# Kernel optimization log

Measured on AMD Instinct MI355X. Metric: run time of the kernel, lower is better.

The kernel has to match this reference:

```python
import jax, jax.numpy as jnp
import numpy as np

N = 100_000      # nodes
E = 1_600_000    # edges
F_IN = 128       # n_features == conv_dim1..3
F_OUT = 256      # concat_dim
G = 2000         # number of graphs in the batch
EPS = 1e-5       # BatchNorm eps


def _xavier(k, shape):
    fan_in, fan_out = shape[-2], shape[-1]
    lim = float(np.sqrt(6.0 / (fan_in + fan_out)))
    return jax.random.uniform(k, shape, jnp.float32, -lim, lim)


def setup_inputs() -> dict:
    key = jax.random.key(0)
    ks = jax.random.split(key, 8)
    x = jax.random.normal(ks[0], (N, F_IN), jnp.float32)
    edge_index = jax.random.randint(ks[1], (2, E), 0, N, dtype=jnp.int64)
    batch = jnp.sort(jax.random.randint(ks[2], (N,), 0, G, dtype=jnp.int64))
    # layers 1..5: F_IN -> F_IN (stacked), layer 6: F_IN -> F_OUT
    Wi = _xavier(ks[3], (5, F_IN, F_IN))   # ARMA init_weight per layer
    Wr = _xavier(ks[4], (5, F_IN, F_IN))   # ARMA root_weight per layer
    b = jnp.zeros((5, F_IN), jnp.float32)  # ARMA bias per layer
    g = jnp.ones((5, F_IN), jnp.float32)   # BN gamma
    be = jnp.zeros((5, F_IN), jnp.float32) # BN beta
    Wi6 = _xavier(ks[5], (F_IN, F_OUT))
    Wr6 = _xavier(ks[6], (F_IN, F_OUT))
    b6 = jnp.zeros((F_OUT,), jnp.float32)
    g6 = jnp.ones((F_OUT,), jnp.float32)
    be6 = jnp.zeros((F_OUT,), jnp.float32)
    return dict(x=x, edge_index=edge_index, batch=batch, Wi=Wi, Wr=Wr, b=b,
                g=g, be=be, Wi6=Wi6, Wr6=Wr6, b6=b6, g6=g6, be6=be6)


def _arma(x, norm, row, col, Wi_l, Wr_l, b_l):
    # ARMAConv (num_stacks=1, num_layers=1, act=ReLU):
    #   out = ReLU( A_norm @ (x W_init) + x W_root + b )
    h = x @ Wi_l                                           # [N, F_out]
    msg = h[row] * norm[:, None]                           # gather + scale, [E, F_out]
    agg = jax.ops.segment_sum(msg, col, num_segments=N)    # scatter-add
    return jax.nn.relu(agg + x @ Wr_l + b_l)


def _bn(x, gamma, beta):
    # BatchNorm1d, training mode (biased batch variance)
    mu = x.mean(axis=0)
    var = x.var(axis=0)
    return gamma * (x - mu) * jax.lax.rsqrt(var + EPS) + beta


def reference(x, edge_index, batch, Wi, Wr, b, g, be, Wi6, Wr6, b6, g6, be6):
    row, col = edge_index[0], edge_index[1]
    # gcn_norm without self loops: D^-1/2 A D^-1/2 edge weights
    deg = jax.ops.segment_sum(jnp.ones((E,), x.dtype), col, num_segments=N)
    dinv = jnp.where(deg > 0, jax.lax.rsqrt(deg), 0.0)
    norm = dinv[row] * dinv[col]                           # [E]

    h = x
    for l in range(5):  # fixed small layer count
        h = _arma(h, norm, row, col, Wi[l], Wr[l], b[l])   # outer F.relu is idempotent
        h = _bn(h, g[l], be[l])
    h = _arma(h, norm, row, col, Wi6, Wr6, b6)
    h = _bn(h, g6, be6)
    # global_add_pool over graph ids; dropout = identity (deterministic baseline)
    out = jax.ops.segment_sum(h, batch, num_segments=G)    # [G, F_OUT]
    return out
```

## Files before the change

### kernel.cpp

```cpp
#include <hip/hip_runtime.h>

#define Nn 100000
#define Ee 1600000
#define Gg 2000
#define EPSf 1e-5f

typedef unsigned short ushort_t;
typedef __attribute__((ext_vector_type(8))) short short8;
typedef __attribute__((ext_vector_type(4))) float f32x4;
typedef __attribute__((ext_vector_type(4))) unsigned u32x4;

__device__ inline float bf2f(unsigned int u) {
    union { unsigned int i; float f; } v; v.i = u << 16; return v.f;
}
__device__ inline unsigned short f2bf(float f) {
    unsigned int x = __float_as_uint(f);
    unsigned int r = (x + 0x7fffu + ((x >> 16) & 1u)) >> 16;
    return (unsigned short)r;
}
__device__ inline int ldidx(const void* a, int i, int i64) {
    return i64 ? (int)((const long long*)a)[i] : ((const int*)a)[i];
}
__device__ inline float ldflt(const void* p, long long i, int f32) {
    return f32 ? ((const float*)p)[i] : bf2f(((const ushort_t*)p)[i]);
}


__global__ void k_flags(const void* gones, const void* ei, int* flags) {
    if (threadIdx.x == 0 && blockIdx.x == 0) {
        unsigned w = *(const unsigned*)gones;
        flags[0] = (w == 0x3F800000u) ? 1 : 0;
        const int* e = (const int*)ei;
        int nz = 0;
        for (int i = 0; i < 256; i++) nz |= e[2 * i + 1];
        flags[1] = nz ? 0 : 1;
    }
}


__global__ void k_hist(const void* __restrict__ ei, int* __restrict__ deg, const int* __restrict__ flags) {
    int i = blockIdx.x * 256 + threadIdx.x;
    if (i < Ee) {
        int c = ldidx(ei, Ee + i, flags[1]);
        atomicAdd(&deg[c], 1);
    }
}

__global__ void k_dinv(const int* __restrict__ deg, float* __restrict__ dinv) {
    int i = blockIdx.x * 256 + threadIdx.x;
    if (i < Nn) { int d = deg[i]; dinv[i] = d > 0 ? rsqrtf((float)d) : 0.f; }
}

__global__ void k_scan1(const int* __restrict__ deg, int* __restrict__ off, int* __restrict__ part) {
    __shared__ int sh[1024];
    int i = blockIdx.x * 1024 + threadIdx.x;
    int v = (i < Nn) ? deg[i] : 0;
    sh[threadIdx.x] = v;
    __syncthreads();
    for (int ofs = 1; ofs < 1024; ofs <<= 1) {
        int t = 0;
        if ((int)threadIdx.x >= ofs) t = sh[threadIdx.x - ofs];
        __syncthreads();
        sh[threadIdx.x] += t;
        __syncthreads();
    }
    if (i < Nn) off[i] = sh[threadIdx.x] - v;
    if (threadIdx.x == 1023) part[blockIdx.x] = sh[1023];
}

__global__ void k_scan2(int* part, int nb) {
    if (threadIdx.x == 0 && blockIdx.x == 0) {
        int run = 0;
        for (int i = 0; i < nb; i++) { int t = part[i]; part[i] = run; run += t; }
    }
}

__global__ void k_scan3(int* __restrict__ off, const int* __restrict__ part, int* __restrict__ cursor) {
    int i = blockIdx.x * 256 + threadIdx.x;
    if (i < Nn) {
        int v = off[i] + part[i >> 10];
        off[i] = v;
        cursor[i] = v;
    }
    if (i == 0) off[Nn] = Ee;
}

__global__ void k_fillp(const void* __restrict__ ei, int* __restrict__ cursor,
                        int* __restrict__ srcS, const int* __restrict__ flags) {
    int range = blockIdx.x & 7;
    int e = (blockIdx.x >> 3) * 256 + threadIdx.x;
    if (e < Ee) {
        int i64 = flags[1];
        int c = ldidx(ei, Ee + e, i64);
        if (c >= range * 12500 && c < (range + 1) * 12500) {
            int r = ldidx(ei, e, i64);
            int p = atomicAdd(&cursor[c], 1);
            srcS[p] = r;
        }
    }
}


__global__ void k_cvt(const void* __restrict__ src, float* __restrict__ dst, int n, const int* __restrict__ flags) {
    int i = blockIdx.x * 256 + threadIdx.x;
    if (i < n) dst[i] = ldflt(src, i, flags[0]);
}

__global__ void k_cvtx(const void* __restrict__ x, ushort_t* __restrict__ xq, const int* __restrict__ flags) {
    int node = blockIdx.x * 256 + threadIdx.x;
    int fc = blockIdx.y;
    if (node < Nn) {
        union { ushort_t u[16]; u32x4 v[2]; } t;
        if (flags[0]) {
            const float* p = (const float*)x + (size_t)node * 128 + fc * 16;
#pragma unroll
            for (int j = 0; j < 16; j++) t.u[j] = f2bf(p[j]);
        } else {
            const ushort_t* p = (const ushort_t*)x + (size_t)node * 128 + fc * 16;
#pragma unroll
            for (int j = 0; j < 16; j++) t.u[j] = p[j];
        }
        u32x4* d = (u32x4*)(xq + ((size_t)fc * Nn + node) * 16);
        d[0] = t.v[0]; d[1] = t.v[1];
    }
}

__global__ void k_pack(const void* __restrict__ Wi, const void* __restrict__ Wr,
                       const void* __restrict__ Wi6, const void* __restrict__ Wr6,
                       ushort_t* __restrict__ Bp, const int* __restrict__ flags) {
    int idx = blockIdx.x * 256 + threadIdx.x;
    if (idx >= 229376) return;
    int f32 = flags[0];
    if (idx < 163840) {
        int l = idx / 32768, rem = idx - l * 32768;
        int kg = rem / 2048, rem2 = rem - kg * 2048;
        int n = rem2 / 8, j = rem2 - n * 8;
        int k = kg * 8 + j;
        float v = (n < 128) ? ldflt(Wi, (l * 128 + k) * 128 + n, f32)
                            : ldflt(Wr, (l * 128 + k) * 128 + (n - 128), f32);
        Bp[idx] = f2bf(v);
    } else {
        int idx2 = idx - 163840;
        int kg = idx2 / 4096, rem2 = idx2 - kg * 4096;
        int n = rem2 / 8, j = rem2 - n * 8;
        int k = kg * 8 + j;
        float v = (n < 256) ? ldflt(Wi6, k * 256 + n, f32) : ldflt(Wr6, k * 256 + (n - 256), f32);
        Bp[idx] = f2bf(v);
    }
}

__global__ void k_fold(const ushort_t* __restrict__ Bp, const float* __restrict__ s,
                       const float* __restrict__ h, const float* __restrict__ bias,
                       ushort_t* __restrict__ Bp2, float* __restrict__ hcorr, int ncat) {
    __shared__ float red[128];
    int n = blockIdx.x, k = threadIdx.x;
    int fhalf = ncat >> 1;
    size_t idx = ((size_t)(k >> 3) * ncat + n) * 8 + (k & 7);
    float w = bf2f(Bp[idx]);
    Bp2[idx] = f2bf(w * s[k]);
    red[k] = h[k] * w;
    __syncthreads();
    for (int m = 64; m > 0; m >>= 1) { if (k < m) red[k] += red[k + m]; __syncthreads(); }
    if (k == 0) hcorr[n] = red[0] + (n >= fhalf ? bias[n - fhalf] : 0.f);
}

__global__ void k_h0(const float* __restrict__ bias, float* __restrict__ hc, int ncat) {
    int n = blockIdx.x * 256 + threadIdx.x;
    if (n < ncat) hc[n] = n >= (ncat >> 1) ? bias[n - (ncat >> 1)] : 0.f;
}


__global__ __launch_bounds__(256) void k_gemm(
        const ushort_t* __restrict__ Aq,
        const ushort_t* __restrict__ Bp, const float* __restrict__ hcorr,
        const float* __restrict__ dinv,
        ushort_t* __restrict__ Hi, ushort_t* __restrict__ yq, int ncat) {
    __shared__ ushort_t As[8448];
    const int tid = threadIdx.x, lane = tid & 63, wid = tid >> 6;
    const int row0 = blockIdx.x * 64;
    const int fhalf = ncat >> 1;

    {
        int node = row0 + lane;
#pragma unroll
        for (int i = 0; i < 4; i++) {
            int kg = wid * 4 + i;
            short8 t;
            if (node < Nn)
                t = *(const short8*)(Aq + ((size_t)(kg >> 1) * Nn + node) * 16 + (kg & 1) * 8);
            else {
#pragma unroll
                for (int j = 0; j < 8; j++) ((ushort_t*)&t)[j] = 0;
            }
            *(short8*)&As[(kg * 64 + lane) * 8] = t;
        }
    }
    __syncthreads();

    const int q = lane >> 4, l15 = lane & 15;
    const int wcL = wid * 64;

    f32x4 acc[4][4];
    f32x4 z; z.x = 0.f; z.y = 0.f; z.z = 0.f; z.w = 0.f;
#pragma unroll
    for (int rt = 0; rt < 4; rt++)
#pragma unroll
        for (int ct = 0; ct < 4; ct++) acc[rt][ct] = z;

#pragma unroll
    for (int kk = 0; kk < 4; kk++) {
        short8 af[4], bfr[4];
        int kg = kk * 4 + q;
#pragma unroll
        for (int rt = 0; rt < 4; rt++)
            af[rt] = *(const short8*)&As[((kg * 64) + rt * 16 + l15) * 8];
#pragma unroll
        for (int ct = 0; ct < 4; ct++) {
            int n = blockIdx.y * 256 + wcL + ct * 16 + l15;
            bfr[ct] = *(const short8*)(Bp + ((size_t)kg * ncat + n) * 8);
        }
#pragma unroll
        for (int rt = 0; rt < 4; rt++)
#pragma unroll
            for (int ct = 0; ct < 4; ct++)
                acc[rt][ct] = __builtin_amdgcn_mfma_f32_16x16x32_bf16(af[rt], bfr[ct], acc[rt][ct], 0, 0, 0);
    }

    ushort_t* stage = As;
#pragma unroll
    for (int half = 0; half < 2; half++) {
        __syncthreads();
#pragma unroll
        for (int ct = 0; ct < 4; ct++) {
            int lcol = wcL + ct * 16 + l15;
            int gcol = blockIdx.y * 256 + lcol;
            float hc = hcorr[gcol];
            bool isHi = gcol < fhalf;
#pragma unroll
            for (int rt2 = 0; rt2 < 2; rt2++) {
                int rt = half * 2 + rt2;
#pragma unroll
                for (int r = 0; r < 4; r++) {
                    int grow = row0 + rt * 16 + q * 4 + r;
                    int gr = grow < Nn ? grow : 0;
                    float v = acc[rt][ct][r] + hc;
                    if (isHi) v *= dinv[gr];
                    stage[(rt2 * 16 + q * 4 + r) * 264 + lcol] = f2bf(v);
                }
            }
        }
        __syncthreads();
        for (int chunk = tid; chunk < 512; chunk += 256) {
            int cg = chunk & 15, rl = chunk >> 4;
            int node = row0 + half * 32 + rl;
            if (node < Nn) {
                int gc0 = blockIdx.y * 256 + cg * 16;
                const u32x4* sp = (const u32x4*)&stage[rl * 264 + cg * 16];
                u32x4 v0 = sp[0], v1 = sp[1];
                ushort_t* dst = (gc0 < fhalf)
                    ? Hi + ((size_t)(gc0 >> 4) * Nn + node) * 16
                    : yq + ((size_t)((gc0 - fhalf) >> 4) * Nn + node) * 16;
                u32x4* dp = (u32x4*)dst;
                dp[0] = v0; dp[1] = v1;
            }
        }
    }
}


__global__ __launch_bounds__(256) void k_agg7(const int* __restrict__ off, const int* __restrict__ src,
                                              const float* __restrict__ dinv, const unsigned* __restrict__ Hi2,
                                              unsigned* __restrict__ yq, float* __restrict__ stat,
                                              int F, int fcbase) {
    const int tid = threadIdx.x;
    const int w = tid >> 6, lane = tid & 63;
    const int sub = lane >> 3, fl = lane & 7;
    const int fc = fcbase + (blockIdx.x & 7);
    const int T = blockIdx.x >> 3;
    const unsigned* __restrict__ base = Hi2 + (size_t)fc * (Nn * 8) + fl;
    float st0 = 0.f, st1 = 0.f, st2 = 0.f, st3 = 0.f;

#pragma unroll
    for (int pass = 0; pass < 4; pass++) {
        int node = T * 128 + pass * 32 + w * 8 + sub;
        bool valid = node < Nn;
        int p0 = 0, p1 = 0;
        if (valid) { p0 = off[node]; p1 = off[node + 1]; }
        float a0 = 0.f, a1 = 0.f;
        int p = p0;
        for (; p + 3 < p1; p += 4) {
            int s0 = src[p], s1 = src[p + 1], s2 = src[p + 2], s3 = src[p + 3];
            unsigned u0 = base[(unsigned)s0 * 8u];
            unsigned u1 = base[(unsigned)s1 * 8u];
            unsigned u2 = base[(unsigned)s2 * 8u];
            unsigned u3 = base[(unsigned)s3 * 8u];
            a0 += bf2f(u0 & 0xffffu); a1 += bf2f(u0 >> 16);
            a0 += bf2f(u1 & 0xffffu); a1 += bf2f(u1 >> 16);
            a0 += bf2f(u2 & 0xffffu); a1 += bf2f(u2 >> 16);
            a0 += bf2f(u3 & 0xffffu); a1 += bf2f(u3 >> 16);
        }
        for (; p < p1; p++) {
            int s0 = src[p];
            unsigned u0 = base[(unsigned)s0 * 8u];
            a0 += bf2f(u0 & 0xffffu); a1 += bf2f(u0 >> 16);
        }
        if (valid) {
            float dv = dinv[node];
            unsigned* yp = yq + ((size_t)fc * Nn + node) * 8 + fl;
            unsigned uv = *yp;
            float vx = fmaxf(bf2f(uv & 0xffffu) + dv * a0, 0.f);
            float vy = fmaxf(bf2f(uv >> 16) + dv * a1, 0.f);
            *yp = (unsigned)f2bf(vx) | ((unsigned)f2bf(vy) << 16);
            st0 += vx; st1 += vx * vx;
            st2 += vy; st3 += vy * vy;
        }
    }
#pragma unroll
    for (int m = 8; m <= 32; m <<= 1) {
        st0 += __shfl_xor(st0, m, 64);
        st1 += __shfl_xor(st1, m, 64);
        st2 += __shfl_xor(st2, m, 64);
        st3 += __shfl_xor(st3, m, 64);
    }
    __shared__ float red[4][8][4];
    if (sub == 0) {
        red[w][fl][0] = st0; red[w][fl][1] = st1;
        red[w][fl][2] = st2; red[w][fl][3] = st3;
    }
    __syncthreads();
    if (tid < 32) {
        int rfl = tid >> 2, k = tid & 3;
        float s = red[0][rfl][k] + red[1][rfl][k] + red[2][rfl][k] + red[3][rfl][k];
        int f = fc * 16 + rfl * 2 + (k >> 1);
        atomicAdd(&stat[(k & 1) * F + f], s);
    }
}


__global__ void k_bnp(const float* __restrict__ stat, const float* __restrict__ gamma,
                      const float* __restrict__ beta, float* __restrict__ scale,
                      float* __restrict__ shift, int F) {
    int f = threadIdx.x;
    if (f < F) {
        float mu = stat[f] * (1.f / Nn);
        float var = stat[F + f] * (1.f / Nn) - mu * mu;
        float rs = rsqrtf(var + EPSf);
        float sc = gamma[f] * rs;
        scale[f] = sc;
        shift[f] = beta[f] - sc * mu;
    }
}


__device__ inline int lb(const void* a, int n, int key, int i64) {
    int lo = 0, hi = n;
    while (lo < hi) { int mid = (lo + hi) >> 1; if (ldidx(a, mid, i64) < key) lo = mid + 1; else hi = mid; }
    return lo;
}

__global__ void k_pool(const ushort_t* __restrict__ y6q, const float* __restrict__ stat,
                       const float* __restrict__ g6, const float* __restrict__ be6,
                       const void* __restrict__ batch, void* __restrict__ out,
                       const int* __restrict__ flags) {
    int g = blockIdx.x;
    int f = threadIdx.x;
    int i64 = flags[1];
    int start = lb(batch, Nn, g, i64);
    int end = lb(batch, Nn, g + 1, i64);
    const ushort_t* yp = y6q + (size_t)(f >> 4) * Nn * 16 + (f & 15);
    float s = 0.f;
    for (int n = start; n < end; n++) s += bf2f(yp[(size_t)n * 16]);
    int cnt = end - start;
    float mu = stat[f] * (1.f / Nn);
    float var = stat[256 + f] * (1.f / Nn) - mu * mu;
    float rs = rsqrtf(var + EPSf);
    float val = g6[f] * rs * (s - (float)cnt * mu) + (float)cnt * be6[f];
    if (flags[0]) ((float*)out)[(size_t)g * 256 + f] = val;
    else          ((ushort_t*)out)[(size_t)g * 256 + f] = f2bf(val);
}


extern "C" void kernel_launch(void* const* d_in, const int* in_sizes, int n_in,
                              void* d_out, int out_size, void* d_ws, size_t ws_size,
                              hipStream_t stream) {
    const void* x    = d_in[0];
    const void* ei   = d_in[1];
    const void* batch= d_in[2];
    const void* Wi   = d_in[3];
    const void* Wr   = d_in[4];
    const void* b    = d_in[5];
    const void* g    = d_in[6];
    const void* be   = d_in[7];
    const void* Wi6  = d_in[8];
    const void* Wr6  = d_in[9];
    const void* b6   = d_in[10];
    const void* g6   = d_in[11];
    const void* be6  = d_in[12];

    char* p = (char*)d_ws;
    auto alloc = [&](size_t bytes) { char* r = p; p += (bytes + 511) & ~(size_t)511; return r; };
    ushort_t* HiB  = (ushort_t*)alloc((size_t)Nn * 256 * 2);
    ushort_t* xq   = (ushort_t*)alloc((size_t)Nn * 128 * 2);
    ushort_t* yAq  = (ushort_t*)alloc((size_t)Nn * 128 * 2);
    ushort_t* yBq  = (ushort_t*)alloc((size_t)Nn * 128 * 2);
    ushort_t* y6q  = (ushort_t*)alloc((size_t)Nn * 256 * 2);
    int* srcS      = (int*)alloc((size_t)Ee * 4);
    int* off       = (int*)alloc((size_t)(Nn + 1) * 4);
    int* cursor    = (int*)alloc((size_t)Nn * 4);
    int* deg       = (int*)alloc((size_t)Nn * 4);
    float* dinv    = (float*)alloc((size_t)Nn * 4);
    int* part      = (int*)alloc(128 * 4);
    float* statsA  = (float*)alloc(6 * 512 * 4);
    float* scaleB  = (float*)alloc(256 * 4);
    float* shiftB  = (float*)alloc(256 * 4);
    ushort_t* Bp   = (ushort_t*)alloc(229376 * 2);
    ushort_t* Bp2  = (ushort_t*)alloc(65536 * 2);
    float* hcorrA  = (float*)alloc(512 * 4);
    int* flags     = (int*)alloc(2 * 4);
    float* biasF   = (float*)alloc(896 * 4);
    float* gF      = (float*)alloc(896 * 4);
    float* beF     = (float*)alloc(896 * 4);
    const unsigned* Hi2 = (const unsigned*)HiB;

    const int AGG_GRID = 782 * 8;

    k_flags<<<1, 64, 0, stream>>>(g, ei, flags);
    k_cvt<<<3, 256, 0, stream>>>(b,  biasF,       640, flags);
    k_cvt<<<1, 256, 0, stream>>>(b6, biasF + 640, 256, flags);
    k_cvt<<<3, 256, 0, stream>>>(g,  gF,          640, flags);
    k_cvt<<<1, 256, 0, stream>>>(g6, gF + 640,    256, flags);
    k_cvt<<<3, 256, 0, stream>>>(be, beF,         640, flags);
    k_cvt<<<1, 256, 0, stream>>>(be6, beF + 640,  256, flags);

    hipMemsetAsync(deg, 0, (size_t)Nn * 4, stream);
    hipMemsetAsync(statsA, 0, 6 * 512 * 4, stream);
    k_hist<<<6250, 256, 0, stream>>>(ei, deg, flags);
    k_dinv<<<391, 256, 0, stream>>>(deg, dinv);
    k_scan1<<<98, 1024, 0, stream>>>(deg, off, part);
    k_scan2<<<1, 64, 0, stream>>>(part, 98);
    k_scan3<<<391, 256, 0, stream>>>(off, part, cursor);
    k_fillp<<<50000, 256, 0, stream>>>(ei, cursor, srcS, flags);
    k_pack<<<896, 256, 0, stream>>>(Wi, Wr, Wi6, Wr6, Bp, flags);
    k_cvtx<<<dim3(391, 8), 256, 0, stream>>>(x, xq, flags);
    k_h0<<<1, 256, 0, stream>>>(biasF, hcorrA, 256);

    k_gemm<<<dim3(1563, 1), 256, 0, stream>>>(xq, Bp, hcorrA, dinv, HiB, yAq, 256);
    k_agg7<<<AGG_GRID, 256, 0, stream>>>(off, srcS, dinv, Hi2, (unsigned*)yAq, statsA, 128, 0);
    k_bnp<<<1, 128, 0, stream>>>(statsA, gF, beF, scaleB, shiftB, 128);
    k_fold<<<256, 128, 0, stream>>>(Bp + 32768, scaleB, shiftB, biasF + 128, Bp2, hcorrA, 256);

    k_gemm<<<dim3(1563, 1), 256, 0, stream>>>(yAq, Bp2, hcorrA, dinv, HiB, yBq, 256);
    k_agg7<<<AGG_GRID, 256, 0, stream>>>(off, srcS, dinv, Hi2, (unsigned*)yBq, statsA + 512, 128, 0);
    k_bnp<<<1, 128, 0, stream>>>(statsA + 512, gF + 128, beF + 128, scaleB, shiftB, 128);
    k_fold<<<256, 128, 0, stream>>>(Bp + 65536, scaleB, shiftB, biasF + 256, Bp2, hcorrA, 256);

    k_gemm<<<dim3(1563, 1), 256, 0, stream>>>(yBq, Bp2, hcorrA, dinv, HiB, yAq, 256);
    k_agg7<<<AGG_GRID, 256, 0, stream>>>(off, srcS, dinv, Hi2, (unsigned*)yAq, statsA + 1024, 128, 0);
    k_bnp<<<1, 128, 0, stream>>>(statsA + 1024, gF + 256, beF + 256, scaleB, shiftB, 128);
    k_fold<<<256, 128, 0, stream>>>(Bp + 98304, scaleB, shiftB, biasF + 384, Bp2, hcorrA, 256);

    k_gemm<<<dim3(1563, 1), 256, 0, stream>>>(yAq, Bp2, hcorrA, dinv, HiB, yBq, 256);
    k_agg7<<<AGG_GRID, 256, 0, stream>>>(off, srcS, dinv, Hi2, (unsigned*)yBq, statsA + 1536, 128, 0);
    k_bnp<<<1, 128, 0, stream>>>(statsA + 1536, gF + 384, beF + 384, scaleB, shiftB, 128);
    k_fold<<<256, 128, 0, stream>>>(Bp + 131072, scaleB, shiftB, biasF + 512, Bp2, hcorrA, 256);

    k_gemm<<<dim3(1563, 1), 256, 0, stream>>>(yBq, Bp2, hcorrA, dinv, HiB, yAq, 256);
    k_agg7<<<AGG_GRID, 256, 0, stream>>>(off, srcS, dinv, Hi2, (unsigned*)yAq, statsA + 2048, 128, 0);
    k_bnp<<<1, 128, 0, stream>>>(statsA + 2048, gF + 512, beF + 512, scaleB, shiftB, 128);
    k_fold<<<512, 128, 0, stream>>>(Bp + 163840, scaleB, shiftB, biasF + 640, Bp2, hcorrA, 512);

    k_gemm<<<dim3(1563, 2), 256, 0, stream>>>(yAq, Bp2, hcorrA, dinv, HiB, y6q, 512);
    k_agg7<<<AGG_GRID, 256, 0, stream>>>(off, srcS, dinv, Hi2, (unsigned*)y6q, statsA + 2560, 256, 0);
    k_agg7<<<AGG_GRID, 256, 0, stream>>>(off, srcS, dinv, Hi2, (unsigned*)y6q, statsA + 2560, 256, 8);
    k_pool<<<Gg, 256, 0, stream>>>(y6q, statsA + 2560, gF + 640, beF + 640, batch, d_out, flags);
}
```

Baseline: 1.330 ms.

## Pad CSR rows to multiples of four with a zero sentinel row for vectorised aggregation

Each node's neighbour list in the CSR is rounded up to a multiple of four, and the padding slots point at an extra all-zero sentinel row appended to the H buffer. This lets the aggregation kernel read source indices as aligned int4 vectors, unroll by eight, and drop the scalar tail loop. The last layer's two aggregation launches become a single launch over all 16 feature chunks. The cost is extra padded edges that gather the zero row, plus setup kernels for padding and zeroing.

```diff
diff --git a/kernel.cpp b/kernel.cpp
--- a/kernel.cpp
+++ b/kernel.cpp
@@ -1,6 +1,7 @@
 #include <hip/hip_runtime.h>
 
 #define Nn 100000
+#define NP 100001
 #define Ee 1600000
 #define Gg 2000
 #define EPSf 1e-5f
@@ -54,7 +55,7 @@
 __global__ void k_scan1(const int* __restrict__ deg, int* __restrict__ off, int* __restrict__ part) {
     __shared__ int sh[1024];
     int i = blockIdx.x * 1024 + threadIdx.x;
-    int v = (i < Nn) ? deg[i] : 0;
+    int v = (i < Nn) ? ((deg[i] + 3) & ~3) : 0;
     sh[threadIdx.x] = v;
     __syncthreads();
     for (int ofs = 1; ofs < 1024; ofs <<= 1) {
@@ -72,6 +73,7 @@
     if (threadIdx.x == 0 && blockIdx.x == 0) {
         int run = 0;
         for (int i = 0; i < nb; i++) { int t = part[i]; part[i] = run; run += t; }
+        part[nb] = run;
     }
 }
 
@@ -82,7 +84,7 @@
         off[i] = v;
         cursor[i] = v;
     }
-    if (i == 0) off[Nn] = Ee;
+    if (i == 0) off[Nn] = part[98];
 }
 
 __global__ void k_fillp(const void* __restrict__ ei, int* __restrict__ cursor,
@@ -98,6 +100,21 @@
             srcS[p] = r;
         }
     }
+}
+
+__global__ void k_pad(const int* __restrict__ cursor, const int* __restrict__ off,
+                      int* __restrict__ srcS) {
+    int i = blockIdx.x * 256 + threadIdx.x;
+    if (i < Nn) {
+        int e = off[i + 1];
+        for (int p = cursor[i]; p < e; p++) srcS[p] = Nn;
+    }
+}
+
+__global__ void k_zrow(ushort_t* __restrict__ Hi) {
+    int t = threadIdx.x;
+    int fc = t >> 4, j = t & 15;
+    Hi[((size_t)fc * NP + Nn) * 16 + j] = 0;
 }
 
 
@@ -258,7 +275,7 @@
                 const u32x4* sp = (const u32x4*)&stage[rl * 264 + cg * 16];
                 u32x4 v0 = sp[0], v1 = sp[1];
                 ushort_t* dst = (gc0 < fhalf)
-                    ? Hi + ((size_t)(gc0 >> 4) * Nn + node) * 16
+                    ? Hi + ((size_t)(gc0 >> 4) * NP + node) * 16
                     : yq + ((size_t)((gc0 - fhalf) >> 4) * Nn + node) * 16;
                 u32x4* dp = (u32x4*)dst;
                 dp[0] = v0; dp[1] = v1;
@@ -268,16 +285,16 @@
 }
 
 
-__global__ __launch_bounds__(256) void k_agg7(const int* __restrict__ off, const int* __restrict__ src,
+__global__ __launch_bounds__(256) void k_agg8(const int* __restrict__ off, const int* __restrict__ src,
                                               const float* __restrict__ dinv, const unsigned* __restrict__ Hi2,
                                               unsigned* __restrict__ yq, float* __restrict__ stat,
-                                              int F, int fcbase) {
+                                              int F, int smask, int sshift) {
     const int tid = threadIdx.x;
     const int w = tid >> 6, lane = tid & 63;
     const int sub = lane >> 3, fl = lane & 7;
-    const int fc = fcbase + (blockIdx.x & 7);
-    const int T = blockIdx.x >> 3;
-    const unsigned* __restrict__ base = Hi2 + (size_t)fc * (Nn * 8) + fl;
+    const int fc = blockIdx.x & smask;
+    const int T = blockIdx.x >> sshift;
+    const unsigned* __restrict__ base = Hi2 + (size_t)fc * (NP * 8) + fl;
     float st0 = 0.f, st1 = 0.f, st2 = 0.f, st3 = 0.f;
 
 #pragma unroll
@@ -288,21 +305,36 @@
         if (valid) { p0 = off[node]; p1 = off[node + 1]; }
         float a0 = 0.f, a1 = 0.f;
         int p = p0;
-        for (; p + 3 < p1; p += 4) {
-            int s0 = src[p], s1 = src[p + 1], s2 = src[p + 2], s3 = src[p + 3];
-            unsigned u0 = base[(unsigned)s0 * 8u];
-            unsigned u1 = base[(unsigned)s1 * 8u];
-            unsigned u2 = base[(unsigned)s2 * 8u];
-            unsigned u3 = base[(unsigned)s3 * 8u];
+        for (; p + 7 < p1; p += 8) {
+            int4 sv0 = *(const int4*)(src + p);
+            int4 sv1 = *(const int4*)(src + p + 4);
+            unsigned u0 = base[(unsigned)sv0.x * 8u];
+            unsigned u1 = base[(unsigned)sv0.y * 8u];
+            unsigned u2 = base[(unsigned)sv0.z * 8u];
+            unsigned u3 = base[(unsigned)sv0.w * 8u];
+            unsigned u4 = base[(unsigned)sv1.x * 8u];
+            unsigned u5 = base[(unsigned)sv1.y * 8u];
+            unsigned u6 = base[(unsigned)sv1.z * 8u];
+            unsigned u7 = base[(unsigned)sv1.w * 8u];
             a0 += bf2f(u0 & 0xffffu); a1 += bf2f(u0 >> 16);
             a0 += bf2f(u1 & 0xffffu); a1 += bf2f(u1 >> 16);
             a0 += bf2f(u2 & 0xffffu); a1 += bf2f(u2 >> 16);
             a0 += bf2f(u3 & 0xffffu); a1 += bf2f(u3 >> 16);
-        }
-        for (; p < p1; p++) {
-            int s0 = src[p];
-            unsigned u0 = base[(unsigned)s0 * 8u];
+            a0 += bf2f(u4 & 0xffffu); a1 += bf2f(u4 >> 16);
+            a0 += bf2f(u5 & 0xffffu); a1 += bf2f(u5 >> 16);
+            a0 += bf2f(u6 & 0xffffu); a1 += bf2f(u6 >> 16);
+            a0 += bf2f(u7 & 0xffffu); a1 += bf2f(u7 >> 16);
+        }
+        if (p < p1) {
+            int4 sv0 = *(const int4*)(src + p);
+            unsigned u0 = base[(unsigned)sv0.x * 8u];
+            unsigned u1 = base[(unsigned)sv0.y * 8u];
+            unsigned u2 = base[(unsigned)sv0.z * 8u];
+            unsigned u3 = base[(unsigned)sv0.w * 8u];
             a0 += bf2f(u0 & 0xffffu); a1 += bf2f(u0 >> 16);
+            a0 += bf2f(u1 & 0xffffu); a1 += bf2f(u1 >> 16);
+            a0 += bf2f(u2 & 0xffffu); a1 += bf2f(u2 >> 16);
+            a0 += bf2f(u3 & 0xffffu); a1 += bf2f(u3 >> 16);
         }
         if (valid) {
             float dv = dinv[node];
@@ -399,12 +431,12 @@
 
     char* p = (char*)d_ws;
     auto alloc = [&](size_t bytes) { char* r = p; p += (bytes + 511) & ~(size_t)511; return r; };
-    ushort_t* HiB  = (ushort_t*)alloc((size_t)Nn * 256 * 2);
+    ushort_t* HiB  = (ushort_t*)alloc((size_t)NP * 256 * 2);
     ushort_t* xq   = (ushort_t*)alloc((size_t)Nn * 128 * 2);
     ushort_t* yAq  = (ushort_t*)alloc((size_t)Nn * 128 * 2);
     ushort_t* yBq  = (ushort_t*)alloc((size_t)Nn * 128 * 2);
     ushort_t* y6q  = (ushort_t*)alloc((size_t)Nn * 256 * 2);
-    int* srcS      = (int*)alloc((size_t)Ee * 4);
+    int* srcS      = (int*)alloc(((size_t)Ee + 4 * Nn + 64) * 4);
     int* off       = (int*)alloc((size_t)(Nn + 1) * 4);
     int* cursor    = (int*)alloc((size_t)Nn * 4);
     int* deg       = (int*)alloc((size_t)Nn * 4);
@@ -440,37 +472,38 @@
     k_scan2<<<1, 64, 0, stream>>>(part, 98);
     k_scan3<<<391, 256, 0, stream>>>(off, part, cursor);
     k_fillp<<<50000, 256, 0, stream>>>(ei, cursor, srcS, flags);
+    k_pad<<<391, 256, 0, stream>>>(cursor, off, srcS);
+    k_zrow<<<1, 256, 0, stream>>>(HiB);
     k_pack<<<896, 256, 0, stream>>>(Wi, Wr, Wi6, Wr6, Bp, flags);
     k_cvtx<<<dim3(391, 8), 256, 0, stream>>>(x, xq, flags);
     k_h0<<<1, 256, 0, stream>>>(biasF, hcorrA, 256);
 
     k_gemm<<<dim3(1563, 1), 256, 0, stream>>>(xq, Bp, hcorrA, dinv, HiB, yAq, 256);
-    k_agg7<<<AGG_GRID, 256, 0, stream>>>(off, srcS, dinv, Hi2, (unsigned*)yAq, statsA, 128, 0);
+    k_agg8<<<AGG_GRID, 256, 0, stream>>>(off, srcS, dinv, Hi2, (unsigned*)yAq, statsA, 128, 7, 3);
     k_bnp<<<1, 128, 0, stream>>>(statsA, gF, beF, scaleB, shiftB, 128);
     k_fold<<<256, 128, 0, stream>>>(Bp + 32768, scaleB, shiftB, biasF + 128, Bp2, hcorrA, 256);
 
     k_gemm<<<dim3(1563, 1), 256, 0, stream>>>(yAq, Bp2, hcorrA, dinv, HiB, yBq, 256);
-    k_agg7<<<AGG_GRID, 256, 0, stream>>>(off, srcS, dinv, Hi2, (unsigned*)yBq, statsA + 512, 128, 0);
+    k_agg8<<<AGG_GRID, 256, 0, stream>>>(off, srcS, dinv, Hi2, (unsigned*)yBq, statsA + 512, 128, 7, 3);
     k_bnp<<<1, 128, 0, stream>>>(statsA + 512, gF + 128, beF + 128, scaleB, shiftB, 128);
     k_fold<<<256, 128, 0, stream>>>(Bp + 65536, scaleB, shiftB, biasF + 256, Bp2, hcorrA, 256);
 
     k_gemm<<<dim3(1563, 1), 256, 0, stream>>>(yBq, Bp2, hcorrA, dinv, HiB, yAq, 256);
-    k_agg7<<<AGG_GRID, 256, 0, stream>>>(off, srcS, dinv, Hi2, (unsigned*)yAq, statsA + 1024, 128, 0);
+    k_agg8<<<AGG_GRID, 256, 0, stream>>>(off, srcS, dinv, Hi2, (unsigned*)yAq, statsA + 1024, 128, 7, 3);
     k_bnp<<<1, 128, 0, stream>>>(statsA + 1024, gF + 256, beF + 256, scaleB, shiftB, 128);
     k_fold<<<256, 128, 0, stream>>>(Bp + 98304, scaleB, shiftB, biasF + 384, Bp2, hcorrA, 256);
 
     k_gemm<<<dim3(1563, 1), 256, 0, stream>>>(yAq, Bp2, hcorrA, dinv, HiB, yBq, 256);
-    k_agg7<<<AGG_GRID, 256, 0, stream>>>(off, srcS, dinv, Hi2, (unsigned*)yBq, statsA + 1536, 128, 0);
+    k_agg8<<<AGG_GRID, 256, 0, stream>>>(off, srcS, dinv, Hi2, (unsigned*)yBq, statsA + 1536, 128, 7, 3);
     k_bnp<<<1, 128, 0, stream>>>(statsA + 1536, gF + 384, beF + 384, scaleB, shiftB, 128);
     k_fold<<<256, 128, 0, stream>>>(Bp + 131072, scaleB, shiftB, biasF + 512, Bp2, hcorrA, 256);
 
     k_gemm<<<dim3(1563, 1), 256, 0, stream>>>(yBq, Bp2, hcorrA, dinv, HiB, yAq, 256);
-    k_agg7<<<AGG_GRID, 256, 0, stream>>>(off, srcS, dinv, Hi2, (unsigned*)yAq, statsA + 2048, 128, 0);
+    k_agg8<<<AGG_GRID, 256, 0, stream>>>(off, srcS, dinv, Hi2, (unsigned*)yAq, statsA + 2048, 128, 7, 3);
     k_bnp<<<1, 128, 0, stream>>>(statsA + 2048, gF + 512, beF + 512, scaleB, shiftB, 128);
     k_fold<<<512, 128, 0, stream>>>(Bp + 163840, scaleB, shiftB, biasF + 640, Bp2, hcorrA, 512);
 
     k_gemm<<<dim3(1563, 2), 256, 0, stream>>>(yAq, Bp2, hcorrA, dinv, HiB, y6q, 512);
-    k_agg7<<<AGG_GRID, 256, 0, stream>>>(off, srcS, dinv, Hi2, (unsigned*)y6q, statsA + 2560, 256, 0);
-    k_agg7<<<AGG_GRID, 256, 0, stream>>>(off, srcS, dinv, Hi2, (unsigned*)y6q, statsA + 2560, 256, 8);
+    k_agg8<<<782 * 16, 256, 0, stream>>>(off, srcS, dinv, Hi2, (unsigned*)y6q, statsA + 2560, 256, 15, 4);
     k_pool<<<Gg, 256, 0, stream>>>(y6q, statsA + 2560, gF + 640, beF + 640, batch, d_out, flags);
 }
```

After: 1.237 ms. -7.0%, faster.
